# Performance work log

Measured on AMD Instinct MI355X. Metric: run time of the kernel, lower is better.

## Reference

```python
import jax, jax.numpy as jnp
import numpy as np

N = 10000      # nodes
E = 160000     # edges (avg degree 16)
H = 128        # hidden_size
L = 3          # n_layers
NRBF = 20
RADIUS = 5.0
EPS = 1e-8
MAXZ = 100


def _xav(k, shape):
    fan_in = shape[-2]
    return jax.random.normal(k, shape, jnp.float32) / jnp.sqrt(jnp.float32(fan_in))


def setup_inputs() -> dict:
    key = jax.random.key(0)
    ks = jax.random.split(key, 12)
    return {
        "z": jax.random.randint(ks[0], (N,), 0, MAXZ, dtype=jnp.int32),
        "edge_vec": jax.random.normal(ks[1], (E, 3), jnp.float32),
        "senders": jax.random.randint(ks[2], (E,), 0, N, dtype=jnp.int32),
        "receivers": jax.random.randint(ks[3], (E,), 0, N, dtype=jnp.int32),
        "emb": jax.random.uniform(ks[4], (MAXZ, H), jnp.float32, -0.1, 0.1),
        "filt_W": _xav(ks[5], (NRBF, L * 3 * H)),
        "filt_b": jnp.zeros((L * 3 * H,), jnp.float32),
        "iW1": _xav(ks[6], (L, H, H)),
        "ib1": jnp.zeros((L, H), jnp.float32),
        "iW2": _xav(ks[7], (L, H, 3 * H)),
        "ib2": jnp.zeros((L, 3 * H), jnp.float32),
        "mW1": _xav(ks[8], (L, 2 * H, H)),
        "mb1": jnp.zeros((L, H), jnp.float32),
        "mW2": _xav(ks[9], (L, H, 3 * H)),
        "mb2": jnp.zeros((L, 3 * H), jnp.float32),
        "vW": _xav(ks[10], (L, H, 2 * H)),
    }


def _painn(z, edge_vec, senders, receivers, emb, filt_W, filt_b,
           iW1, ib1, iW2, ib2, mW1, mb1, mW2, mb2, vW):
    n = z.shape[0]
    clip = lambda x: jnp.clip(x, -1e4, 1e4)

    # edge geometry: norm + direction
    d = jnp.sqrt(jnp.sum(edge_vec ** 2, axis=-1, keepdims=True) + EPS)  # [E,1]
    dir_ij = edge_vec / d                                               # [E,3]

    # gaussian radial basis + cosine cutoff
    mu = jnp.linspace(0.0, RADIUS, NRBF)
    gamma = 0.5 / (RADIUS / NRBF) ** 2
    phi = jnp.exp(-gamma * (d - mu) ** 2)                               # [E,NRBF]
    cut = 0.5 * (jnp.cos(jnp.pi * d / RADIUS) + 1.0) * (d < RADIUS)     # [E,1]

    filters = (phi @ filt_W + filt_b) * cut                             # [E, L*3H]
    filt = jnp.split(filters, L, axis=-1)

    # embed
    s = emb[z]                                                          # [N,H]
    v = jnp.zeros((n, 3, H), dtype=s.dtype)                             # [N,3,H]

    for l in range(L):
        # ---- message ----
        x = jax.nn.silu(s @ iW1[l] + ib1[l]) @ iW2[l] + ib2[l]          # [N,3H]
        m = filt[l] * x[receivers]                                      # [E,3H]
        ds, dv1, dv2 = jnp.split(m, 3, axis=-1)
        dv = dv1[:, None, :] * dir_ij[:, :, None] + dv2[:, None, :] * v[receivers]  # [E,3,H]
        ds = jax.ops.segment_sum(ds, senders, num_segments=n)
        dv = jax.ops.segment_sum(dv, senders, num_segments=n)
        s = s + clip(ds)
        v = v + clip(dv)
        # ---- update / mixing ----
        v_l, v_r = jnp.split(v @ vW[l], 2, axis=-1)                     # [N,3,H] each
        v_norm = jnp.sqrt(jnp.sum(v_l ** 2, axis=-2) + EPS)             # [N,H]
        ts = jnp.concatenate([s, v_norm], axis=-1)                      # [N,2H]
        mm = jax.nn.silu(ts @ mW1[l] + mb1[l]) @ mW2[l] + mb2[l]        # [N,3H]
        ds2, dvu, dsv = jnp.split(mm, 3, axis=-1)
        s = s + clip(ds2 + dsv * jnp.sum(v_l * v_r, axis=1))
        v = v + clip(dvu[:, None, :] * v_r)
    return s, v


def reference(z, edge_vec, senders, receivers, emb, filt_W, filt_b,
              iW1, ib1, iW2, ib2, mW1, mb1, mW2, mb2, vW):
    return _painn(z, edge_vec, senders, receivers, emb, filt_W, filt_b,
                  iW1, ib1, iW2, ib2, mW1, mb1, mW2, mb2, vW)
```

## Files before the change

kernel.cpp:

```cpp
#include <hip/hip_runtime.h>
#include <math.h>

#define NN 10000
#define EE 160000
#define H 128
#define LAYERS 3
#define NRBF 20
#define RADIUS 5.0f
#define PI_F 3.14159265358979323846f

using f16    = _Float16;
using h2     = __attribute__((ext_vector_type(2)))  _Float16;
using half8  = __attribute__((ext_vector_type(8)))  _Float16;
using f32x16 = __attribute__((ext_vector_type(16))) float;
using u32x4  = __attribute__((ext_vector_type(4)))  unsigned int;

__device__ __forceinline__ float clipf(float x){ return fminf(fmaxf(x, -1e4f), 1e4f); }
__device__ __forceinline__ float siluf(float x){ return x / (1.0f + __expf(-x)); }

__global__ __launch_bounds__(256) void hist_kernel(const int* __restrict__ send, int* __restrict__ cnt){
    int e = blockIdx.x * 256 + threadIdx.x;
    if (e < EE) atomicAdd(&cnt[send[e]], 1);
}

__global__ __launch_bounds__(1024) void scan_kernel(const int* __restrict__ cnt,
                                                    int* __restrict__ row_ptr,
                                                    int* __restrict__ cursor){
    __shared__ int part[1024];
    int t = threadIdx.x;
    int base = t * 10;
    int local[10];
    int sum = 0;
    #pragma unroll
    for (int i = 0; i < 10; i++){
        int idx = base + i;
        local[i] = (idx < NN) ? cnt[idx] : 0;
        sum += local[i];
    }
    part[t] = sum;
    __syncthreads();
    for (int off = 1; off < 1024; off <<= 1){
        int val = (t >= off) ? part[t - off] : 0;
        __syncthreads();
        part[t] += val;
        __syncthreads();
    }
    int run = (t > 0) ? part[t-1] : 0;
    #pragma unroll
    for (int i = 0; i < 10; i++){
        int idx = base + i;
        if (idx < NN){ row_ptr[idx] = run; cursor[idx] = run; run += local[i]; }
    }
    if (t == 1023) row_ptr[NN] = part[1023];
}

__global__ __launch_bounds__(256) void build_kernel(const float* __restrict__ ev,
                                                    const int* __restrict__ send,
                                                    const int* __restrict__ recv,
                                                    int* __restrict__ cursor,
                                                    int* __restrict__ recv_s,
                                                    f16* __restrict__ Ps){
    int e = blockIdx.x * 256 + threadIdx.x;
    if (e >= EE) return;
    int p = atomicAdd(&cursor[send[e]], 1);
    recv_s[p] = recv[e];
    float x = ev[e*3+0], y = ev[e*3+1], z = ev[e*3+2];
    float d = sqrtf(x*x + y*y + z*z + 1e-8f);
    float inv = 1.0f / d;
    float cut = (d < RADIUS) ? 0.5f * (__cosf(PI_F * d / RADIUS) + 1.0f) : 0.0f;
    union { u32x4 q[3]; f16 h[24]; } o;
    #pragma unroll
    for (int k = 0; k < NRBF; k++){
        float mu = RADIUS * (float)k / (float)(NRBF - 1);
        float t = d - mu;
        o.h[k] = (f16)(__expf(-8.0f * t * t) * cut);
    }
    o.h[20] = (f16)cut;
    o.h[21] = (f16)(x*inv); o.h[22] = (f16)(y*inv); o.h[23] = (f16)(z*inv);
    u32x4* dst = (u32x4*)(Ps + (size_t)p*24);
    dst[0] = o.q[0]; dst[1] = o.q[1]; dst[2] = o.q[2];
}

__global__ __launch_bounds__(256) void wconv_kernel(const float* __restrict__ iW1, const float* __restrict__ iW2,
                                                    const float* __restrict__ vW,  const float* __restrict__ mW1,
                                                    const float* __restrict__ mW2,
                                                    f16* __restrict__ iW1T, f16* __restrict__ iW2T,
                                                    f16* __restrict__ vWT,  f16* __restrict__ mW1T,
                                                    f16* __restrict__ mW2T){
    int idx = blockIdx.x*256 + threadIdx.x;
    if (idx >= 3*180224) return;
    int l = idx / 180224;
    int r = idx % 180224;
    float val; f16* dst;
    if (r < 16384){
        int n = r >> 7, k = r & 127;
        val = iW1[l*16384 + k*128 + n]; dst = iW1T + l*16384 + r;
    } else if (r < 65536){
        int r2 = r - 16384; int n = r2 >> 7, k = r2 & 127;
        val = iW2[l*49152 + k*384 + n]; dst = iW2T + l*49152 + r2;
    } else if (r < 98304){
        int r2 = r - 65536; int n = r2 >> 7, k = r2 & 127;
        val = vW[l*32768 + k*256 + n]; dst = vWT + l*32768 + r2;
    } else if (r < 131072){
        int r2 = r - 98304; int n = r2 >> 8, k = r2 & 255;
        val = mW1[l*32768 + k*128 + n]; dst = mW1T + l*32768 + r2;
    } else {
        int r2 = r - 131072; int n = r2 >> 7, k = r2 & 127;
        val = mW2[l*49152 + k*384 + n]; dst = mW2T + l*49152 + r2;
    }
    *dst = (f16)val;
}

__global__ __launch_bounds__(256) void embed_kernel(const int* __restrict__ z,
                                                    const float* __restrict__ emb,
                                                    float* __restrict__ s, f16* __restrict__ sh){
    int idx = blockIdx.x * 256 + threadIdx.x;
    if (idx >= NN * H) return;
    int n = idx >> 7, h = idx & 127;
    float val = emb[z[n]*H + h];
    s[idx] = val;
    sh[idx] = (f16)val;
}

template<int K, int NTOT, bool SILU, bool BIAS, int MODE, typename OT>
__global__ __launch_bounds__(256) void mgemm_kernel(const f16* __restrict__ A,
                                                    const f16* __restrict__ A2,
                                                    const f16* __restrict__ WT,
                                                    const float* __restrict__ bias,
                                                    OT* __restrict__ out, int M){
    __shared__ f16 As[64][K+8];
    int t = threadIdx.x;
    int n0 = blockIdx.x * 64;
    {
        int row = t >> 2;
        int seg0 = (t & 3) * (K/4);
        bool valid = (n0 + row) < M;
        #pragma unroll
        for (int j = 0; j < K/32; j++){
            int k = seg0 + j*8;
            half8 val = {};
            if (valid){
                if (MODE == 0) val = *(const half8*)(A + (size_t)(n0+row)*K + k);
                else {
                    const f16* base = (k < 128) ? A : A2;
                    int ko = k & 127;
                    val = *(const half8*)(base + (size_t)(n0+row)*128 + ko);
                }
            }
            *(half8*)&As[row][k] = val;
        }
    }
    __syncthreads();
    int lane = t & 63, w = t >> 6;
    int wr = w >> 1, wc = w & 1;
    int arow = wr*32 + (lane & 31);
    int bcol = blockIdx.y*64 + wc*32 + (lane & 31);
    int koff = (lane >> 5) * 8;
    const f16* ap = &As[arow][koff];
    const f16* bp = WT + (size_t)bcol*K + koff;
    f32x16 acc = {};
    #pragma unroll
    for (int kc = 0; kc < K/16; kc++){
        half8 af = *(const half8*)(ap + kc*16);
        half8 bf = *(const half8*)(bp + kc*16);
        acc = __builtin_amdgcn_mfma_f32_32x32x16_f16(af, bf, acc, 0, 0, 0);
    }
    float bv = BIAS ? bias[bcol] : 0.0f;
    int rbase = n0 + wr*32 + 4*(lane>>5);
    #pragma unroll
    for (int r = 0; r < 16; r++){
        int row = rbase + (r&3) + 8*(r>>2);
        if (row < M){
            float val = acc[r] + bv;
            if (SILU) val = siluf(val);
            out[(size_t)row*NTOT + bcol] = (OT)val;
        }
    }
}

template<int K1, bool CONCAT>
__global__ __launch_bounds__(256) void mlp_kernel(const f16* __restrict__ A,
                                                  const f16* __restrict__ A2,
                                                  const f16* __restrict__ W1T,
                                                  const float* __restrict__ b1,
                                                  const f16* __restrict__ W2T,
                                                  const float* __restrict__ b2,
                                                  f16* __restrict__ out, int M){
    __shared__ f16 As[64][K1+8];
    __shared__ f16 Hs[64][136];
    int t = threadIdx.x;
    int n0 = blockIdx.x * 64;
    {
        int row = t >> 2;
        int seg0 = (t & 3) * (K1/4);
        bool valid = (n0 + row) < M;
        #pragma unroll
        for (int j = 0; j < K1/32; j++){
            int k = seg0 + j*8;
            half8 val = {};
            if (valid){
                if (!CONCAT) val = *(const half8*)(A + (size_t)(n0+row)*K1 + k);
                else {
                    const f16* base = (k < 128) ? A : A2;
                    val = *(const half8*)(base + (size_t)(n0+row)*128 + (k & 127));
                }
            }
            *(half8*)&As[row][k] = val;
        }
    }
    __syncthreads();
    int lane = t & 63, w = t >> 6;
    int koff = (lane >> 5) * 8;
    int ar = lane & 31;
    {
        int bcol = w*32 + (lane & 31);
        const f16* bp = W1T + (size_t)bcol*K1 + koff;
        f32x16 acc0 = {}, acc1 = {};
        #pragma unroll
        for (int kc = 0; kc < K1/16; kc++){
            half8 bf = *(const half8*)(bp + kc*16);
            half8 a0 = *(const half8*)(&As[ar][koff + kc*16]);
            half8 a1 = *(const half8*)(&As[32+ar][koff + kc*16]);
            acc0 = __builtin_amdgcn_mfma_f32_32x32x16_f16(a0, bf, acc0, 0, 0, 0);
            acc1 = __builtin_amdgcn_mfma_f32_32x32x16_f16(a1, bf, acc1, 0, 0, 0);
        }
        float bv = b1[bcol];
        #pragma unroll
        for (int r = 0; r < 16; r++){
            int row = (r&3) + 8*(r>>2) + 4*(lane>>5);
            Hs[row][bcol]    = (f16)siluf(acc0[r] + bv);
            Hs[32+row][bcol] = (f16)siluf(acc1[r] + bv);
        }
    }
    __syncthreads();
    #pragma unroll
    for (int cc = 0; cc < 3; cc++){
        int bcol = (w + cc*4)*32 + (lane & 31);
        const f16* bp = W2T + (size_t)bcol*128 + koff;
        f32x16 acc0 = {}, acc1 = {};
        #pragma unroll
        for (int kc = 0; kc < 8; kc++){
            half8 bf = *(const half8*)(bp + kc*16);
            half8 a0 = *(const half8*)(&Hs[ar][koff + kc*16]);
            half8 a1 = *(const half8*)(&Hs[32+ar][koff + kc*16]);
            acc0 = __builtin_amdgcn_mfma_f32_32x32x16_f16(a0, bf, acc0, 0, 0, 0);
            acc1 = __builtin_amdgcn_mfma_f32_32x32x16_f16(a1, bf, acc1, 0, 0, 0);
        }
        float bv = b2[bcol];
        #pragma unroll
        for (int r = 0; r < 16; r++){
            int row = (r&3) + 8*(r>>2) + 4*(lane>>5);
            int g0 = n0 + row, g1 = n0 + 32 + row;
            if (g0 < M) out[(size_t)g0*384 + bcol] = (f16)(acc0[r] + bv);
            if (g1 < M) out[(size_t)g1*384 + bcol] = (f16)(acc1[r] + bv);
        }
    }
}

__global__ __launch_bounds__(256) void msg_kernel(const f16* __restrict__ Ps,
                                                  const int* __restrict__ recv_s,
                                                  const int* __restrict__ row_ptr,
                                                  const f16* __restrict__ xh,
                                                  const f16* __restrict__ vh,
                                                  const float* __restrict__ fW, const float* __restrict__ fb,
                                                  float* __restrict__ s, f16* __restrict__ sh,
                                                  float* __restrict__ v, f16* __restrict__ v2h, int l){
    int t = threadIdx.x;
    int lane = t & 63;
    int n = blockIdx.x * 4 + (t >> 6);
    int h0 = lane * 2;
    int col0 = l*384 + h0;
    h2 wf0[NRBF], wf1[NRBF], wf2[NRBF];
    #pragma unroll
    for (int k = 0; k < NRBF; k++){
        const float* w = fW + k*1152 + col0;
        wf0[k] = h2{(f16)w[0],   (f16)w[1]};
        wf1[k] = h2{(f16)w[128], (f16)w[129]};
        wf2[k] = h2{(f16)w[256], (f16)w[257]};
    }
    float b0x = fb[col0],     b0y = fb[col0+1];
    float b1x = fb[col0+128], b1y = fb[col0+129];
    float b2x = fb[col0+256], b2y = fb[col0+257];
    int beg = row_ptr[n], end = row_ptr[n+1];
    float ds0=0.f, ds1=0.f, dv00=0.f, dv01=0.f, dv10=0.f, dv11=0.f, dv20=0.f, dv21=0.f;
    #pragma unroll 2
    for (int idx = beg; idx < end; idx++){
        const u32x4* pp = (const u32x4*)(Ps + (size_t)idx*24);
        union { u32x4 q[3]; f16 ph[24]; } u;
        u.q[0] = pp[0]; u.q[1] = pp[1]; u.q[2] = pp[2];
        int r = recv_s[idx];
        h2 f0 = {}, f1 = {}, f2 = {};
        #pragma unroll
        for (int k = 0; k < NRBF; k++){
            f16 pk = u.ph[k];
            h2 pk2 = h2{pk, pk};
            f0 += pk2 * wf0[k];
            f1 += pk2 * wf1[k];
            f2 += pk2 * wf2[k];
        }
        float cut = (float)u.ph[20];
        float F00 = fmaf(b0x, cut, (float)f0.x), F01 = fmaf(b0y, cut, (float)f0.y);
        float F10 = fmaf(b1x, cut, (float)f1.x), F11 = fmaf(b1y, cut, (float)f1.y);
        float F20 = fmaf(b2x, cut, (float)f2.x), F21 = fmaf(b2y, cut, (float)f2.y);
        const f16* xr = xh + (size_t)r*384 + h0;
        h2 X0 = *(const h2*)xr;
        h2 X1 = *(const h2*)(xr + 128);
        h2 X2 = *(const h2*)(xr + 256);
        const f16* vp = vh + (size_t)r*384 + h0;
        h2 V0 = *(const h2*)vp;
        h2 V1 = *(const h2*)(vp + 128);
        h2 V2 = *(const h2*)(vp + 256);
        float d0 = (float)u.ph[21], d1 = (float)u.ph[22], d2 = (float)u.ph[23];
        ds0 = fmaf(F00, (float)X0.x, ds0);
        float a0 = F10 * (float)X1.x, bb0 = F20 * (float)X2.x;
        dv00 = fmaf(a0, d0, fmaf(bb0, (float)V0.x, dv00));
        dv10 = fmaf(a0, d1, fmaf(bb0, (float)V1.x, dv10));
        dv20 = fmaf(a0, d2, fmaf(bb0, (float)V2.x, dv20));
        ds1 = fmaf(F01, (float)X0.y, ds1);
        float a1 = F11 * (float)X1.y, bb1 = F21 * (float)X2.y;
        dv01 = fmaf(a1, d0, fmaf(bb1, (float)V0.y, dv01));
        dv11 = fmaf(a1, d1, fmaf(bb1, (float)V1.y, dv11));
        dv21 = fmaf(a1, d2, fmaf(bb1, (float)V2.y, dv21));
    }
    int si = n*H + h0;
    float sv0 = s[si]   + clipf(ds0);
    float sv1 = s[si+1] + clipf(ds1);
    s[si] = sv0; s[si+1] = sv1;
    *(h2*)&sh[si] = h2{(f16)sv0, (f16)sv1};
    size_t vb = (size_t)n*384 + h0;
    float nv00 = v[vb]     + clipf(dv00), nv01 = v[vb+1]   + clipf(dv01);
    float nv10 = v[vb+128] + clipf(dv10), nv11 = v[vb+129] + clipf(dv11);
    float nv20 = v[vb+256] + clipf(dv20), nv21 = v[vb+257] + clipf(dv21);
    v[vb] = nv00;     v[vb+1] = nv01;
    v[vb+128] = nv10; v[vb+129] = nv11;
    v[vb+256] = nv20; v[vb+257] = nv21;
    *(h2*)&v2h[vb]     = h2{(f16)nv00, (f16)nv01};
    *(h2*)&v2h[vb+128] = h2{(f16)nv10, (f16)nv11};
    *(h2*)&v2h[vb+256] = h2{(f16)nv20, (f16)nv21};
}

__global__ __launch_bounds__(256) void u1_kernel(const f16* __restrict__ vlr,
                                                 f16* __restrict__ vnormh, float* __restrict__ dotl){
    int idx = blockIdx.x * 256 + threadIdx.x;
    if (idx >= NN*H) return;
    int n = idx >> 7, h = idx & 127;
    const f16* b = vlr + (size_t)n*768 + h;
    float l0 = (float)b[0],   l1 = (float)b[256], l2 = (float)b[512];
    float r0 = (float)b[128], r1 = (float)b[384], r2 = (float)b[640];
    vnormh[idx] = (f16)sqrtf(l0*l0 + l1*l1 + l2*l2 + 1e-8f);
    dotl[idx]   = l0*r0 + l1*r1 + l2*r2;
}

__global__ __launch_bounds__(256) void u4_kernel(const f16* __restrict__ mm, const float* __restrict__ dotl,
                                                 const f16* __restrict__ vlr,
                                                 float* __restrict__ s, f16* __restrict__ sh,
                                                 float* __restrict__ v, f16* __restrict__ vh){
    int idx = blockIdx.x * 256 + threadIdx.x;
    if (idx >= NN*H) return;
    int n = idx >> 7, h = idx & 127;
    const f16* mp = mm + (size_t)n*384;
    float m0 = (float)mp[h], m1 = (float)mp[128+h], m2 = (float)mp[256+h];
    float sv = s[idx] + clipf(m0 + m2*dotl[idx]);
    s[idx] = sv; sh[idx] = (f16)sv;
    const f16* br = vlr + (size_t)n*768 + 128 + h;
    size_t vb = (size_t)n*384 + h;
    float nv0 = v[vb]     + clipf(m1 * (float)br[0]);
    float nv1 = v[vb+128] + clipf(m1 * (float)br[256]);
    float nv2 = v[vb+256] + clipf(m1 * (float)br[512]);
    v[vb]     = nv0; vh[vb]     = (f16)nv0;
    v[vb+128] = nv1; vh[vb+128] = (f16)nv1;
    v[vb+256] = nv2; vh[vb+256] = (f16)nv2;
}

extern "C" void kernel_launch(void* const* d_in, const int* in_sizes, int n_in,
                              void* d_out, int out_size, void* d_ws, size_t ws_size,
                              hipStream_t stream) {
    const int*   z    = (const int*)  d_in[0];
    const float* ev   = (const float*)d_in[1];
    const int*   send = (const int*)  d_in[2];
    const int*   recv = (const int*)  d_in[3];
    const float* emb  = (const float*)d_in[4];
    const float* fW   = (const float*)d_in[5];
    const float* fb   = (const float*)d_in[6];
    const float* iW1  = (const float*)d_in[7];
    const float* ib1  = (const float*)d_in[8];
    const float* iW2  = (const float*)d_in[9];
    const float* ib2  = (const float*)d_in[10];
    const float* mW1  = (const float*)d_in[11];
    const float* mb1  = (const float*)d_in[12];
    const float* mW2  = (const float*)d_in[13];
    const float* mb2  = (const float*)d_in[14];
    const float* vW   = (const float*)d_in[15];

    float* s = (float*)d_out;
    float* v = s + NN*H;

    char* base = (char*)d_ws;
    f16*   Ps     = (f16*)base;   base += (size_t)EE*24*2;
    int*   recvs  = (int*)base;   base += (size_t)EE*4;
    f16*   xh     = (f16*)base;
    f16*   mmh    = (f16*)base;   base += (size_t)NN*384*2;
    f16*   v2h    = (f16*)base;   base += (size_t)NN*384*2;
    f16*   vh     = (f16*)base;   base += (size_t)NN*384*2;
    f16*   vlr    = (f16*)base;   base += (size_t)NN*768*2;
    f16*   vnormh = (f16*)base;   base += (size_t)NN*128*2;
    float* dotl   = (float*)base; base += (size_t)NN*128*4;
    f16*   sh     = (f16*)base;   base += (size_t)NN*128*2;
    f16*   iW1T   = (f16*)base;   base += (size_t)3*16384*2;
    f16*   iW2T   = (f16*)base;   base += (size_t)3*49152*2;
    f16*   vWT    = (f16*)base;   base += (size_t)3*32768*2;
    f16*   mW1T   = (f16*)base;   base += (size_t)3*32768*2;
    f16*   mW2T   = (f16*)base;   base += (size_t)3*49152*2;
    int* cnt      = (int*)base;   base += (size_t)NN*4;
    int* row_ptr  = (int*)base;   base += (size_t)(NN+1)*4;
    int* cursor   = (int*)base;

    hipMemsetAsync(cnt, 0, NN*sizeof(int), stream);
    hist_kernel<<<(EE+255)/256, 256, 0, stream>>>(send, cnt);
    scan_kernel<<<1, 1024, 0, stream>>>(cnt, row_ptr, cursor);
    build_kernel<<<(EE+255)/256, 256, 0, stream>>>(ev, send, recv, cursor, recvs, Ps);
    wconv_kernel<<<(3*180224+255)/256, 256, 0, stream>>>(iW1, iW2, vW, mW1, mW2,
                                                         iW1T, iW2T, vWT, mW1T, mW2T);
    embed_kernel<<<(NN*H+255)/256, 256, 0, stream>>>(z, emb, s, sh);
    hipMemsetAsync(v, 0, (size_t)NN*384*sizeof(float), stream);
    hipMemsetAsync(vh, 0, (size_t)NN*384*sizeof(f16), stream);

    const int MB  = (NN  + 63) / 64;
    const int MB3 = (3*NN + 63) / 64;

    for (int l = 0; l < LAYERS; l++){
        mlp_kernel<128,false><<<MB, 256, 0, stream>>>(sh, nullptr, iW1T + l*16384, ib1 + l*H,
                                                      iW2T + l*49152, ib2 + l*384, xh, NN);
        msg_kernel<<<NN/4, 256, 0, stream>>>(Ps, recvs, row_ptr, xh, vh, fW, fb, s, sh, v, v2h, l);
        mgemm_kernel<128,256,false,false,0,f16><<<dim3(MB3,4), 256, 0, stream>>>(v2h, nullptr, vWT + l*32768, nullptr, vlr, 3*NN);
        u1_kernel<<<(NN*H + 255)/256, 256, 0, stream>>>(vlr, vnormh, dotl);
        mlp_kernel<256,true><<<MB, 256, 0, stream>>>(sh, vnormh, mW1T + l*32768, mb1 + l*H,
                                                     mW2T + l*49152, mb2 + l*384, mmh, NN);
        u4_kernel<<<(NN*H + 255)/256, 256, 0, stream>>>(mmh, dotl, vlr, s, sh, v, vh);
    }
}
```

Before: 448.9 us.

## Fuse vector-mix GEMM with norm/dot and mixing MLP with update epilogue

Replaces the separate vW GEMM plus u1 reduction with one vlr kernel that computes left/right projections for all three components in registers and emits the norm, dot and v_r directly. The mixing MLP absorbs the u4 update in its epilogue, so the full mm and vlr intermediates no longer go through global memory. The f16 vector buffers move to a component-major layout, and the message kernel drops to 128-thread blocks. This cuts two launches per layer and a lot of intermediate traffic. In exchange it raises register pressure in the fused kernels and reads the input sh while also writing it, which relies on each block touching only its own rows.

```diff
diff --git a/kernel.cpp b/kernel.cpp
--- a/kernel.cpp
+++ b/kernel.cpp
@@ -122,89 +122,25 @@
     sh[idx] = (f16)val;
 }
 
-template<int K, int NTOT, bool SILU, bool BIAS, int MODE, typename OT>
-__global__ __launch_bounds__(256) void mgemm_kernel(const f16* __restrict__ A,
-                                                    const f16* __restrict__ A2,
-                                                    const f16* __restrict__ WT,
-                                                    const float* __restrict__ bias,
-                                                    OT* __restrict__ out, int M){
-    __shared__ f16 As[64][K+8];
-    int t = threadIdx.x;
-    int n0 = blockIdx.x * 64;
-    {
-        int row = t >> 2;
-        int seg0 = (t & 3) * (K/4);
-        bool valid = (n0 + row) < M;
-        #pragma unroll
-        for (int j = 0; j < K/32; j++){
-            int k = seg0 + j*8;
-            half8 val = {};
-            if (valid){
-                if (MODE == 0) val = *(const half8*)(A + (size_t)(n0+row)*K + k);
-                else {
-                    const f16* base = (k < 128) ? A : A2;
-                    int ko = k & 127;
-                    val = *(const half8*)(base + (size_t)(n0+row)*128 + ko);
-                }
-            }
-            *(half8*)&As[row][k] = val;
-        }
-    }
-    __syncthreads();
-    int lane = t & 63, w = t >> 6;
-    int wr = w >> 1, wc = w & 1;
-    int arow = wr*32 + (lane & 31);
-    int bcol = blockIdx.y*64 + wc*32 + (lane & 31);
-    int koff = (lane >> 5) * 8;
-    const f16* ap = &As[arow][koff];
-    const f16* bp = WT + (size_t)bcol*K + koff;
-    f32x16 acc = {};
-    #pragma unroll
-    for (int kc = 0; kc < K/16; kc++){
-        half8 af = *(const half8*)(ap + kc*16);
-        half8 bf = *(const half8*)(bp + kc*16);
-        acc = __builtin_amdgcn_mfma_f32_32x32x16_f16(af, bf, acc, 0, 0, 0);
-    }
-    float bv = BIAS ? bias[bcol] : 0.0f;
-    int rbase = n0 + wr*32 + 4*(lane>>5);
-    #pragma unroll
-    for (int r = 0; r < 16; r++){
-        int row = rbase + (r&3) + 8*(r>>2);
-        if (row < M){
-            float val = acc[r] + bv;
-            if (SILU) val = siluf(val);
-            out[(size_t)row*NTOT + bcol] = (OT)val;
-        }
-    }
-}
-
-template<int K1, bool CONCAT>
-__global__ __launch_bounds__(256) void mlp_kernel(const f16* __restrict__ A,
-                                                  const f16* __restrict__ A2,
-                                                  const f16* __restrict__ W1T,
-                                                  const float* __restrict__ b1,
-                                                  const f16* __restrict__ W2T,
-                                                  const float* __restrict__ b2,
-                                                  f16* __restrict__ out, int M){
-    __shared__ f16 As[64][K1+8];
+__global__ __launch_bounds__(256) void mlp1_kernel(const f16* __restrict__ A,
+                                                   const f16* __restrict__ W1T,
+                                                   const float* __restrict__ b1,
+                                                   const f16* __restrict__ W2T,
+                                                   const float* __restrict__ b2,
+                                                   f16* __restrict__ out){
+    __shared__ f16 As[64][136];
     __shared__ f16 Hs[64][136];
     int t = threadIdx.x;
     int n0 = blockIdx.x * 64;
     {
         int row = t >> 2;
-        int seg0 = (t & 3) * (K1/4);
-        bool valid = (n0 + row) < M;
-        #pragma unroll
-        for (int j = 0; j < K1/32; j++){
+        int seg0 = (t & 3) * 32;
+        bool valid = (n0 + row) < NN;
+        #pragma unroll
+        for (int j = 0; j < 4; j++){
             int k = seg0 + j*8;
             half8 val = {};
-            if (valid){
-                if (!CONCAT) val = *(const half8*)(A + (size_t)(n0+row)*K1 + k);
-                else {
-                    const f16* base = (k < 128) ? A : A2;
-                    val = *(const half8*)(base + (size_t)(n0+row)*128 + (k & 127));
-                }
-            }
+            if (valid) val = *(const half8*)(A + (size_t)(n0+row)*128 + k);
             *(half8*)&As[row][k] = val;
         }
     }
@@ -213,11 +149,11 @@
     int koff = (lane >> 5) * 8;
     int ar = lane & 31;
     {
-        int bcol = w*32 + (lane & 31);
-        const f16* bp = W1T + (size_t)bcol*K1 + koff;
+        int bcol = w*32 + ar;
+        const f16* bp = W1T + (size_t)bcol*128 + koff;
         f32x16 acc0 = {}, acc1 = {};
         #pragma unroll
-        for (int kc = 0; kc < K1/16; kc++){
+        for (int kc = 0; kc < 8; kc++){
             half8 bf = *(const half8*)(bp + kc*16);
             half8 a0 = *(const half8*)(&As[ar][koff + kc*16]);
             half8 a1 = *(const half8*)(&As[32+ar][koff + kc*16]);
@@ -235,7 +171,7 @@
     __syncthreads();
     #pragma unroll
     for (int cc = 0; cc < 3; cc++){
-        int bcol = (w + cc*4)*32 + (lane & 31);
+        int bcol = (w + cc*4)*32 + ar;
         const f16* bp = W2T + (size_t)bcol*128 + koff;
         f32x16 acc0 = {}, acc1 = {};
         #pragma unroll
@@ -251,13 +187,13 @@
         for (int r = 0; r < 16; r++){
             int row = (r&3) + 8*(r>>2) + 4*(lane>>5);
             int g0 = n0 + row, g1 = n0 + 32 + row;
-            if (g0 < M) out[(size_t)g0*384 + bcol] = (f16)(acc0[r] + bv);
-            if (g1 < M) out[(size_t)g1*384 + bcol] = (f16)(acc1[r] + bv);
-        }
-    }
-}
-
-__global__ __launch_bounds__(256) void msg_kernel(const f16* __restrict__ Ps,
+            if (g0 < NN) out[(size_t)g0*384 + bcol] = (f16)(acc0[r] + bv);
+            if (g1 < NN) out[(size_t)g1*384 + bcol] = (f16)(acc1[r] + bv);
+        }
+    }
+}
+
+__global__ __launch_bounds__(128) void msg_kernel(const f16* __restrict__ Ps,
                                                   const int* __restrict__ recv_s,
                                                   const int* __restrict__ row_ptr,
                                                   const f16* __restrict__ xh,
@@ -267,7 +203,7 @@
                                                   float* __restrict__ v, f16* __restrict__ v2h, int l){
     int t = threadIdx.x;
     int lane = t & 63;
-    int n = blockIdx.x * 4 + (t >> 6);
+    int n = blockIdx.x * 2 + (t >> 6);
     int h0 = lane * 2;
     int col0 = l*384 + h0;
     h2 wf0[NRBF], wf1[NRBF], wf2[NRBF];
@@ -306,10 +242,10 @@
         h2 X0 = *(const h2*)xr;
         h2 X1 = *(const h2*)(xr + 128);
         h2 X2 = *(const h2*)(xr + 256);
-        const f16* vp = vh + (size_t)r*384 + h0;
+        const f16* vp = vh + (size_t)r*128 + h0;
         h2 V0 = *(const h2*)vp;
-        h2 V1 = *(const h2*)(vp + 128);
-        h2 V2 = *(const h2*)(vp + 256);
+        h2 V1 = *(const h2*)(vp + (size_t)NN*128);
+        h2 V2 = *(const h2*)(vp + (size_t)2*NN*128);
         float d0 = (float)u.ph[21], d1 = (float)u.ph[22], d2 = (float)u.ph[23];
         ds0 = fmaf(F00, (float)X0.x, ds0);
         float a0 = F10 * (float)X1.x, bb0 = F20 * (float)X2.x;
@@ -334,42 +270,161 @@
     v[vb] = nv00;     v[vb+1] = nv01;
     v[vb+128] = nv10; v[vb+129] = nv11;
     v[vb+256] = nv20; v[vb+257] = nv21;
-    *(h2*)&v2h[vb]     = h2{(f16)nv00, (f16)nv01};
-    *(h2*)&v2h[vb+128] = h2{(f16)nv10, (f16)nv11};
-    *(h2*)&v2h[vb+256] = h2{(f16)nv20, (f16)nv21};
-}
-
-__global__ __launch_bounds__(256) void u1_kernel(const f16* __restrict__ vlr,
-                                                 f16* __restrict__ vnormh, float* __restrict__ dotl){
-    int idx = blockIdx.x * 256 + threadIdx.x;
-    if (idx >= NN*H) return;
-    int n = idx >> 7, h = idx & 127;
-    const f16* b = vlr + (size_t)n*768 + h;
-    float l0 = (float)b[0],   l1 = (float)b[256], l2 = (float)b[512];
-    float r0 = (float)b[128], r1 = (float)b[384], r2 = (float)b[640];
-    vnormh[idx] = (f16)sqrtf(l0*l0 + l1*l1 + l2*l2 + 1e-8f);
-    dotl[idx]   = l0*r0 + l1*r1 + l2*r2;
-}
-
-__global__ __launch_bounds__(256) void u4_kernel(const f16* __restrict__ mm, const float* __restrict__ dotl,
-                                                 const f16* __restrict__ vlr,
-                                                 float* __restrict__ s, f16* __restrict__ sh,
-                                                 float* __restrict__ v, f16* __restrict__ vh){
-    int idx = blockIdx.x * 256 + threadIdx.x;
-    if (idx >= NN*H) return;
-    int n = idx >> 7, h = idx & 127;
-    const f16* mp = mm + (size_t)n*384;
-    float m0 = (float)mp[h], m1 = (float)mp[128+h], m2 = (float)mp[256+h];
-    float sv = s[idx] + clipf(m0 + m2*dotl[idx]);
-    s[idx] = sv; sh[idx] = (f16)sv;
-    const f16* br = vlr + (size_t)n*768 + 128 + h;
-    size_t vb = (size_t)n*384 + h;
-    float nv0 = v[vb]     + clipf(m1 * (float)br[0]);
-    float nv1 = v[vb+128] + clipf(m1 * (float)br[256]);
-    float nv2 = v[vb+256] + clipf(m1 * (float)br[512]);
-    v[vb]     = nv0; vh[vb]     = (f16)nv0;
-    v[vb+128] = nv1; vh[vb+128] = (f16)nv1;
-    v[vb+256] = nv2; vh[vb+256] = (f16)nv2;
+    size_t pb = (size_t)n*128 + h0;
+    *(h2*)&v2h[pb]                    = h2{(f16)nv00, (f16)nv01};
+    *(h2*)&v2h[pb + (size_t)NN*128]   = h2{(f16)nv10, (f16)nv11};
+    *(h2*)&v2h[pb + (size_t)2*NN*128] = h2{(f16)nv20, (f16)nv21};
+}
+
+__global__ __launch_bounds__(256) void vlr_kernel(const f16* __restrict__ v2h,
+                                                  const f16* __restrict__ vWT,
+                                                  f16* __restrict__ vrh,
+                                                  f16* __restrict__ vnormh,
+                                                  float* __restrict__ dotl){
+    __shared__ f16 As[3][32][136];
+    int t = threadIdx.x;
+    int n0 = blockIdx.x * 32;
+    for (int i = t; i < 1536; i += 256){
+        int c = i / 512; int rem = i - c*512; int row = rem >> 4; int k8 = (rem & 15) * 8;
+        bool valid = (n0 + row) < NN;
+        half8 val = {};
+        if (valid) val = *(const half8*)(v2h + ((size_t)c*NN + n0 + row)*128 + k8);
+        *(half8*)&As[c][row][k8] = val;
+    }
+    __syncthreads();
+    int lane = t & 63, w = t >> 6;
+    int ar = lane & 31;
+    int koff = (lane >> 5) * 8;
+    int jl = w*32 + ar;
+    half8 Bl[8], Br[8];
+    #pragma unroll
+    for (int kc = 0; kc < 8; kc++){
+        Bl[kc] = *(const half8*)(vWT + (size_t)jl*128 + koff + kc*16);
+        Br[kc] = *(const half8*)(vWT + (size_t)(128+jl)*128 + koff + kc*16);
+    }
+    f32x16 al[3], arr[3];
+    #pragma unroll
+    for (int c = 0; c < 3; c++){
+        f32x16 accl = {}, accr = {};
+        #pragma unroll
+        for (int kc = 0; kc < 8; kc++){
+            half8 a = *(const half8*)(&As[c][ar][koff + kc*16]);
+            accl = __builtin_amdgcn_mfma_f32_32x32x16_f16(a, Bl[kc], accl, 0, 0, 0);
+            accr = __builtin_amdgcn_mfma_f32_32x32x16_f16(a, Br[kc], accr, 0, 0, 0);
+        }
+        al[c] = accl; arr[c] = accr;
+    }
+    #pragma unroll
+    for (int r = 0; r < 16; r++){
+        int node = n0 + (r&3) + 8*(r>>2) + 4*(lane>>5);
+        if (node < NN){
+            float l0=al[0][r], l1=al[1][r], l2=al[2][r];
+            float r0=arr[0][r], r1=arr[1][r], r2=arr[2][r];
+            size_t si = (size_t)node*128 + jl;
+            vnormh[si] = (f16)sqrtf(l0*l0 + l1*l1 + l2*l2 + 1e-8f);
+            dotl[si]   = l0*r0 + l1*r1 + l2*r2;
+            vrh[si]                    = (f16)r0;
+            vrh[si + (size_t)NN*128]   = (f16)r1;
+            vrh[si + (size_t)2*NN*128] = (f16)r2;
+        }
+    }
+}
+
+__global__ __launch_bounds__(256) void mlp2u4_kernel(const f16* __restrict__ shin,
+                                                     const f16* __restrict__ vnormh,
+                                                     const f16* __restrict__ W1T,
+                                                     const float* __restrict__ b1,
+                                                     const f16* __restrict__ W2T,
+                                                     const float* __restrict__ b2,
+                                                     const float* __restrict__ dotl,
+                                                     const f16* __restrict__ vrh,
+                                                     float* __restrict__ s, f16* __restrict__ sh,
+                                                     float* __restrict__ v, f16* __restrict__ vh){
+    __shared__ f16 As[64][264];
+    __shared__ f16 Hs[64][136];
+    int t = threadIdx.x;
+    int n0 = blockIdx.x * 64;
+    {
+        int row = t >> 2;
+        int seg0 = (t & 3) * 64;
+        bool valid = (n0 + row) < NN;
+        #pragma unroll
+        for (int j = 0; j < 8; j++){
+            int k = seg0 + j*8;
+            half8 val = {};
+            if (valid){
+                const f16* base = (k < 128) ? shin : vnormh;
+                val = *(const half8*)(base + (size_t)(n0+row)*128 + (k & 127));
+            }
+            *(half8*)&As[row][k] = val;
+        }
+    }
+    __syncthreads();
+    int lane = t & 63, w = t >> 6;
+    int koff = (lane >> 5) * 8;
+    int ar = lane & 31;
+    {
+        int bcol = w*32 + ar;
+        const f16* bp = W1T + (size_t)bcol*256 + koff;
+        f32x16 acc0 = {}, acc1 = {};
+        #pragma unroll
+        for (int kc = 0; kc < 16; kc++){
+            half8 bf = *(const half8*)(bp + kc*16);
+            half8 a0 = *(const half8*)(&As[ar][koff + kc*16]);
+            half8 a1 = *(const half8*)(&As[32+ar][koff + kc*16]);
+            acc0 = __builtin_amdgcn_mfma_f32_32x32x16_f16(a0, bf, acc0, 0, 0, 0);
+            acc1 = __builtin_amdgcn_mfma_f32_32x32x16_f16(a1, bf, acc1, 0, 0, 0);
+        }
+        float bv = b1[bcol];
+        #pragma unroll
+        for (int r = 0; r < 16; r++){
+            int row = (r&3) + 8*(r>>2) + 4*(lane>>5);
+            Hs[row][bcol]    = (f16)siluf(acc0[r] + bv);
+            Hs[32+row][bcol] = (f16)siluf(acc1[r] + bv);
+        }
+    }
+    __syncthreads();
+    f32x16 acc[3][2];
+    #pragma unroll
+    for (int cc = 0; cc < 3; cc++){
+        int bcol = (w + cc*4)*32 + ar;
+        const f16* bp = W2T + (size_t)bcol*128 + koff;
+        f32x16 a0 = {}, a1 = {};
+        #pragma unroll
+        for (int kc = 0; kc < 8; kc++){
+            half8 bf = *(const half8*)(bp + kc*16);
+            half8 h0v = *(const half8*)(&Hs[ar][koff + kc*16]);
+            half8 h1v = *(const half8*)(&Hs[32+ar][koff + kc*16]);
+            a0 = __builtin_amdgcn_mfma_f32_32x32x16_f16(h0v, bf, a0, 0, 0, 0);
+            a1 = __builtin_amdgcn_mfma_f32_32x32x16_f16(h1v, bf, a1, 0, 0, 0);
+        }
+        acc[cc][0] = a0; acc[cc][1] = a1;
+    }
+    int jj = w*32 + ar;
+    float bv0 = b2[jj], bv1 = b2[128 + jj], bv2 = b2[256 + jj];
+    #pragma unroll
+    for (int rg = 0; rg < 2; rg++){
+        #pragma unroll
+        for (int r = 0; r < 16; r++){
+            int node = n0 + rg*32 + (r&3) + 8*(r>>2) + 4*(lane>>5);
+            if (node < NN){
+                float m0 = acc[0][rg][r] + bv0;
+                float m1 = acc[1][rg][r] + bv1;
+                float m2 = acc[2][rg][r] + bv2;
+                size_t si = (size_t)node*128 + jj;
+                float sv = s[si] + clipf(m0 + m2*dotl[si]);
+                s[si] = sv; sh[si] = (f16)sv;
+                #pragma unroll
+                for (int c = 0; c < 3; c++){
+                    size_t pi = si + (size_t)c*NN*128;
+                    float vrv = (float)vrh[pi];
+                    size_t vi = (size_t)node*384 + c*128 + jj;
+                    float nv = v[vi] + clipf(m1 * vrv);
+                    v[vi] = nv; vh[pi] = (f16)nv;
+                }
+            }
+        }
+    }
 }
 
 extern "C" void kernel_launch(void* const* d_in, const int* in_sizes, int n_in,
@@ -398,11 +453,10 @@
     char* base = (char*)d_ws;
     f16*   Ps     = (f16*)base;   base += (size_t)EE*24*2;
     int*   recvs  = (int*)base;   base += (size_t)EE*4;
-    f16*   xh     = (f16*)base;
-    f16*   mmh    = (f16*)base;   base += (size_t)NN*384*2;
-    f16*   v2h    = (f16*)base;   base += (size_t)NN*384*2;
-    f16*   vh     = (f16*)base;   base += (size_t)NN*384*2;
-    f16*   vlr    = (f16*)base;   base += (size_t)NN*768*2;
+    f16*   xh     = (f16*)base;   base += (size_t)NN*384*2;
+    f16*   v2h    = (f16*)base;   base += (size_t)3*NN*128*2;
+    f16*   vh     = (f16*)base;   base += (size_t)3*NN*128*2;
+    f16*   vrh    = (f16*)base;   base += (size_t)3*NN*128*2;
     f16*   vnormh = (f16*)base;   base += (size_t)NN*128*2;
     float* dotl   = (float*)base; base += (size_t)NN*128*4;
     f16*   sh     = (f16*)base;   base += (size_t)NN*128*2;
@@ -422,20 +476,19 @@
     wconv_kernel<<<(3*180224+255)/256, 256, 0, stream>>>(iW1, iW2, vW, mW1, mW2,
                                                          iW1T, iW2T, vWT, mW1T, mW2T);
     embed_kernel<<<(NN*H+255)/256, 256, 0, stream>>>(z, emb, s, sh);
-    hipMemsetAsync(v, 0, (size_t)NN*384*sizeof(float), stream);
-    hipMemsetAsync(vh, 0, (size_t)NN*384*sizeof(f16), stream);
-
-    const int MB  = (NN  + 63) / 64;
-    const int MB3 = (3*NN + 63) / 64;
+    hipMemsetAsync(v,  0, (size_t)NN*384*sizeof(float), stream);
+    hipMemsetAsync(vh, 0, (size_t)3*NN*128*sizeof(f16), stream);
+
+    const int MB  = (NN + 63) / 64;
+    const int VB  = (NN + 31) / 32;
 
     for (int l = 0; l < LAYERS; l++){
-        mlp_kernel<128,false><<<MB, 256, 0, stream>>>(sh, nullptr, iW1T + l*16384, ib1 + l*H,
-                                                      iW2T + l*49152, ib2 + l*384, xh, NN);
-        msg_kernel<<<NN/4, 256, 0, stream>>>(Ps, recvs, row_ptr, xh, vh, fW, fb, s, sh, v, v2h, l);
-        mgemm_kernel<128,256,false,false,0,f16><<<dim3(MB3,4), 256, 0, stream>>>(v2h, nullptr, vWT + l*32768, nullptr, vlr, 3*NN);
-        u1_kernel<<<(NN*H + 255)/256, 256, 0, stream>>>(vlr, vnormh, dotl);
-        mlp_kernel<256,true><<<MB, 256, 0, stream>>>(sh, vnormh, mW1T + l*32768, mb1 + l*H,
-                                                     mW2T + l*49152, mb2 + l*384, mmh, NN);
-        u4_kernel<<<(NN*H + 255)/256, 256, 0, stream>>>(mmh, dotl, vlr, s, sh, v, vh);
-    }
-}
+        mlp1_kernel<<<MB, 256, 0, stream>>>(sh, iW1T + l*16384, ib1 + l*H,
+                                            iW2T + l*49152, ib2 + l*384, xh);
+        msg_kernel<<<NN/2, 128, 0, stream>>>(Ps, recvs, row_ptr, xh, vh, fW, fb, s, sh, v, v2h, l);
+        vlr_kernel<<<VB, 256, 0, stream>>>(v2h, vWT + l*32768, vrh, vnormh, dotl);
+        mlp2u4_kernel<<<MB, 256, 0, stream>>>(sh, vnormh, mW1T + l*32768, mb1 + l*H,
+                                              mW2T + l*49152, mb2 + l*384,
+                                              dotl, vrh, s, sh, v, vh);
+    }
+}
```

New measurement: 412.3 us. -8.1%, faster.
